# Optimization experiments

Hardware: AMD Instinct MI355X
Metric: run time of the kernel (lower is better)

Reference implementation:

```python
import jax, jax.numpy as jnp
import numpy as np

B, C, N, T = 32, 32, 300, 64      # batch, residual/conv channels, nodes, seq_len
DIM, K, SKIP, GD = 40, 20, 64, 2  # node_dim, top-k (subgraph_size), skip_channels, gcn_depth
TANH_A, PROP_A = 3.0, 0.05
KSET = (2, 3, 6, 7)
TOUT = T - (KSET[-1] - 1)          # 58: time length after dilated inception (dilation=1)


def conv2d(x, w, b):
    y = jax.lax.conv_general_dilated(x, w, (1, 1), 'VALID', dimension_numbers=('NCHW', 'OIHW', 'NCHW'))
    return y + b[None, :, None, None]


def setup_inputs() -> dict:
    key = jax.random.key(0)
    ks = iter(jax.random.split(key, 48))
    def nrm(shape, s=1.0):
        return jax.random.normal(next(ks), shape, jnp.float32) * s
    inp = {
        'x': nrm((B, C, N, T)),
        'x_skip': nrm((B, SKIP, N, 1)),
        'idx': jnp.arange(N, dtype=jnp.int32),
        'emb1': nrm((N, DIM), 0.1), 'emb2': nrm((N, DIM), 0.1),
        'lin1_w': nrm((DIM, DIM), 0.15), 'lin1_b': jnp.zeros((DIM,), jnp.float32),
        'lin2_w': nrm((DIM, DIM), 0.15), 'lin2_b': jnp.zeros((DIM,), jnp.float32),
        'skip_w': nrm((SKIP, C, 1, TOUT), 0.05), 'skip_b': jnp.zeros((SKIP,), jnp.float32),
        'mp1_w': nrm((C, (GD + 1) * C, 1, 1), 0.1), 'mp1_b': jnp.zeros((C,), jnp.float32),
        'mp2_w': nrm((C, (GD + 1) * C, 1, 1), 0.1), 'mp2_b': jnp.zeros((C,), jnp.float32),
        'ln_w': jnp.ones((C, N, TOUT), jnp.float32), 'ln_b': jnp.zeros((C, N, TOUT), jnp.float32),
    }
    for k in KSET:
        inp[f'fw{k}'] = nrm((C // 4, C, 1, k), 0.1); inp[f'fb{k}'] = jnp.zeros((C // 4,), jnp.float32)
        inp[f'gw{k}'] = nrm((C // 4, C, 1, k), 0.1); inp[f'gb{k}'] = jnp.zeros((C // 4,), jnp.float32)
    return inp


def _forward(x, x_skip, idx, emb1, emb2, lin1_w, lin1_b, lin2_w, lin2_b,
             fws, gws, skip_w, skip_b, mp1_w, mp1_b, mp2_w, mp2_b, ln_w, ln_b):
    # --- GraphConstructor: learned sparse adjacency via tanh/relu/top-k/scatter ---
    n1 = jnp.tanh(TANH_A * (emb1[idx] @ lin1_w.T + lin1_b))
    n2 = jnp.tanh(TANH_A * (emb2[idx] @ lin2_w.T + lin2_b))
    a = n1 @ n2.T - n2 @ n1.T
    A = jax.nn.relu(jnp.tanh(TANH_A * a))
    _, cols = jax.lax.top_k(A, K)                               # [N, K] per-row top-k indices
    mask = jnp.zeros_like(A).at[jnp.arange(N)[:, None], cols].set(1.0)
    A = A * mask
    # --- DilatedInception filter/gate (Conv2d kernel (1,k), crop to shortest) ---
    Xf = jnp.tanh(jnp.concatenate([conv2d(x, w, b)[..., -TOUT:] for w, b in fws], axis=1))
    Xg = jax.nn.sigmoid(jnp.concatenate([conv2d(x, w, b)[..., -TOUT:] for w, b in gws], axis=1))
    X = Xf * Xg                                                 # dropout is identity (training=False)
    X_skip_out = conv2d(X, skip_w, skip_b) + x_skip             # [B, SKIP, N, 1]
    # --- MixProp graph diffusion over A and A^T ---
    def mixprop(Xin, Adj, w, b):
        Ah = Adj + jnp.eye(N, dtype=Adj.dtype)
        Ah = Ah / Ah.sum(1)[:, None]                            # row-normalize
        H, hops = Xin, [Xin]
        for _ in range(GD):
            H = PROP_A * Xin + (1.0 - PROP_A) * jnp.einsum('bcwt,vw->bcvt', H, Ah)
            hops.append(H)
        return conv2d(jnp.concatenate(hops, axis=1), w, b)      # 1x1 conv: (GD+1)*C -> C
    X = mixprop(X, A, mp1_w, mp1_b) + mixprop(X, A.T, mp2_w, mp2_b)
    X = X + x[..., -TOUT:]
    # --- LayerNorm over (C, N, TOUT) with node-indexed affine ---
    mu = X.mean(axis=(1, 2, 3), keepdims=True)
    var = ((X - mu) ** 2).mean(axis=(1, 2, 3), keepdims=True)
    Xn = (X - mu) * jax.lax.rsqrt(var + 1e-5)
    X = Xn * ln_w[:, idx, :][None] + ln_b[:, idx, :][None]
    return X, X_skip_out


def reference(x, x_skip, idx, emb1, emb2, lin1_w, lin1_b, lin2_w, lin2_b,
              fw2, fb2, fw3, fb3, fw6, fb6, fw7, fb7,
              gw2, gb2, gw3, gb3, gw6, gb6, gw7, gb7,
              skip_w, skip_b, mp1_w, mp1_b, mp2_w, mp2_b, ln_w, ln_b):
    fws = [(fw2, fb2), (fw3, fb3), (fw6, fb6), (fw7, fb7)]
    gws = [(gw2, gb2), (gw3, gb3), (gw6, gb6), (gw7, gb7)]
    return _forward(x, x_skip, idx, emb1, emb2, lin1_w, lin1_b, lin2_w, lin2_b,
                    fws, gws, skip_w, skip_b, mp1_w, mp1_b, mp2_w, mp2_b, ln_w, ln_b)
```

## Files before the change

### kernel.cpp

```cpp
#include <hip/hip_runtime.h>
#include <hip/hip_bf16.h>
#include <math.h>

typedef __hip_bfloat16 bf16;
typedef __attribute__((ext_vector_type(8))) short bf16x8;
typedef __attribute__((ext_vector_type(4))) float f32x4;

#define NB 32
#define NC 32
#define NNODE 300
#define NT 64
#define NDIM 40
#define KTOP 20
#define NSKIP 64
#define NTOUT 58
#define SLAB 17400
#define BSLAB 556800
#define XEL 17817600
#define PSLAB 2048
#define BPSLAB 614400
#define XPEL 19660800

__device__ __forceinline__ float b2f(bf16 v){ return __bfloat162float(v); }
__device__ __forceinline__ bf16 f2b(float v){ return __float2bfloat16(v); }
__device__ __forceinline__ float fsig(float x){ return 1.0f/(1.0f + __expf(-x)); }
__device__ __forceinline__ float ftanh(float x){ return 2.0f*fsig(2.0f*x) - 1.0f; }

__device__ __forceinline__ unsigned short bbits(float v){
  bf16 h = f2b(v); unsigned short s; __builtin_memcpy(&s, &h, 2); return s;
}

__device__ __forceinline__ void fma8(float acc[8], uint4 d, float vv){
  acc[0] = fmaf(vv, __uint_as_float(d.x << 16),          acc[0]);
  acc[1] = fmaf(vv, __uint_as_float(d.x & 0xffff0000u),  acc[1]);
  acc[2] = fmaf(vv, __uint_as_float(d.y << 16),          acc[2]);
  acc[3] = fmaf(vv, __uint_as_float(d.y & 0xffff0000u),  acc[3]);
  acc[4] = fmaf(vv, __uint_as_float(d.z << 16),          acc[4]);
  acc[5] = fmaf(vv, __uint_as_float(d.z & 0xffff0000u),  acc[5]);
  acc[6] = fmaf(vv, __uint_as_float(d.w << 16),          acc[6]);
  acc[7] = fmaf(vv, __uint_as_float(d.w & 0xffff0000u),  acc[7]);
}

__device__ __forceinline__ void unp8(float f[8], uint4 d){
  f[0] = __uint_as_float(d.x << 16); f[1] = __uint_as_float(d.x & 0xffff0000u);
  f[2] = __uint_as_float(d.y << 16); f[3] = __uint_as_float(d.y & 0xffff0000u);
  f[4] = __uint_as_float(d.z << 16); f[5] = __uint_as_float(d.z & 0xffff0000u);
  f[6] = __uint_as_float(d.w << 16); f[7] = __uint_as_float(d.w & 0xffff0000u);
}

__device__ __forceinline__ uint4 pack8(const float f[8]){
  uint4 d;
  d.x = (unsigned)bbits(f[0]) | ((unsigned)bbits(f[1]) << 16);
  d.y = (unsigned)bbits(f[2]) | ((unsigned)bbits(f[3]) << 16);
  d.z = (unsigned)bbits(f[4]) | ((unsigned)bbits(f[5]) << 16);
  d.w = (unsigned)bbits(f[6]) | ((unsigned)bbits(f[7]) << 16);
  return d;
}

__device__ __forceinline__ void bv_swz(int bid, int& b, int& v){
  int xcd = bid & 7, i = bid >> 3;
  int nb = xcd*1200 + i;
  b = nb / NNODE; v = nb - b*NNODE;
}

__global__ void k_nodes(const float* __restrict__ emb1, const float* __restrict__ emb2,
                        const float* __restrict__ l1w, const float* __restrict__ l1b,
                        const float* __restrict__ l2w, const float* __restrict__ l2b,
                        const int* __restrict__ idxp,
                        float* __restrict__ n1, float* __restrict__ n2){
  int i = blockIdx.x; int d = threadIdx.x;
  if (d >= NDIM) return;
  int r = idxp[i];
  float a1 = l1b[d], a2 = l2b[d];
  for (int k=0;k<NDIM;++k){
    a1 = fmaf(emb1[r*NDIM+k], l1w[d*NDIM+k], a1);
    a2 = fmaf(emb2[r*NDIM+k], l2w[d*NDIM+k], a2);
  }
  n1[i*NDIM+d] = tanhf(3.0f*a1);
  n2[i*NDIM+d] = tanhf(3.0f*a2);
}

__global__ void __launch_bounds__(64) k_adjrow(const float* __restrict__ n1,
                                               const float* __restrict__ n2,
                                               float* __restrict__ Am){
  int i = blockIdx.x; int lane = threadIdx.x;
  __shared__ float rowo[NNODE];
  __shared__ float rowv[NNODE];
  __shared__ int   sel[NNODE];
  for (int j=lane;j<NNODE;j+=64){
    float a = 0.f;
    #pragma unroll
    for (int k=0;k<NDIM;++k){
      float a1 = n1[i*NDIM+k], a2 = n2[i*NDIM+k];
      a = fmaf(a1, n2[j*NDIM+k], a);
      a = fmaf(-a2, n1[j*NDIM+k], a);
    }
    float v = tanhf(3.0f*a);
    v = v > 0.f ? v : 0.f;
    rowo[j]=v; rowv[j]=v; sel[j]=0;
  }
  __syncthreads();
  for (int it=0; it<KTOP; ++it){
    float best = -1.f; int bi = 0x7fffffff;
    for (int j=lane;j<NNODE;j+=64){
      float v = rowv[j];
      if (v > best){ best=v; bi=j; }
    }
    #pragma unroll
    for (int off=32; off; off>>=1){
      float ov = __shfl_xor(best, off);
      int   oi = __shfl_xor(bi, off);
      if (ov > best || (ov == best && oi < bi)){ best=ov; bi=oi; }
    }
    if (lane==0){ sel[bi]=1; rowv[bi]=-2.f; }
    __syncthreads();
  }
  for (int j=lane;j<NNODE;j+=64)
    Am[i*NNODE+j] = sel[j] ? rowo[j] : 0.f;
}

__global__ void __launch_bounds__(64) k_csr(const float* __restrict__ Am,
                                            int* __restrict__ aidx, float* __restrict__ aval,
                                            int* __restrict__ acnt){
  int r = blockIdx.x; int lane = threadIdx.x;
  int v = (r < NNODE) ? r : r - NNODE;
  int*   ip = aidx + r*304;
  float* vp = aval + r*304;
  if (lane==0){ ip[0]=v; vp[0]=1.0f; }
  int cnt = 1; float s = 1.0f;
  for (int base=0; base<NNODE; base+=64){
    int j = base + lane; float val = 0.f; bool p = false;
    if (j < NNODE){
      val = (r < NNODE) ? Am[v*NNODE + j] : Am[j*NNODE + v];
      p = val > 0.f;
    }
    unsigned long long m = __ballot(p);
    int pre = __popcll(m & ((1ull << lane) - 1ull));
    if (p){ ip[cnt+pre]=j; vp[cnt+pre]=val; }
    cnt += __popcll(m);
    float vs = p ? val : 0.f;
    #pragma unroll
    for (int off=32; off; off>>=1) vs += __shfl_xor(vs, off);
    s += vs;
  }
  for (int e=lane; e<cnt; e+=64) vp[e] = vp[e] / s;
  if (lane==0) acnt[r]=cnt;
}

__global__ void k_wpack2(const float* __restrict__ fw2,const float* __restrict__ fw3,
                         const float* __restrict__ fw6,const float* __restrict__ fw7,
                         const float* __restrict__ gw2,const float* __restrict__ gw3,
                         const float* __restrict__ gw6,const float* __restrict__ gw7,
                         const float* __restrict__ fb2,const float* __restrict__ fb3,
                         const float* __restrict__ fb6,const float* __restrict__ fb7,
                         const float* __restrict__ gb2,const float* __restrict__ gb3,
                         const float* __restrict__ gb6,const float* __restrict__ gb7,
                         bf16* __restrict__ wfA, float* __restrict__ biasPk){
  int T = blockIdx.x*blockDim.x + threadIdx.x;
  if (T < 14336){
    int j = T & 7;
    int q = T >> 3;
    int l = q & 63; q >>= 6;
    int ks = q % 7, mt = q / 7;
    int m = mt*16 + (l & 15);
    int k = ks*32 + (l >> 4)*8 + j;
    int c = m >> 1, path = m & 1;
    int cls = c >> 3, o = c & 7;
    int ic = k / 7, d = k - ic*7;
    int kk = (cls==0) ? 2 : (cls==1) ? 3 : (cls==2) ? 6 : 7;
    int tp = d - (7 - kk);
    float val = 0.f;
    if (tp >= 0){
      const float* w = (path==0)
        ? (cls==0?fw2:cls==1?fw3:cls==2?fw6:fw7)
        : (cls==0?gw2:cls==1?gw3:cls==2?gw6:gw7);
      val = w[(o*NC + ic)*kk + tp];
    }
    wfA[T] = f2b(val);
  } else if (T < 14336 + 32){
    int c = T - 14336;
    int cls = c >> 3, o = c & 7;
    const float* fb = cls==0?fb2:cls==1?fb3:cls==2?fb6:fb7;
    const float* gb = cls==0?gb2:cls==1?gb3:cls==2?gb6:gb7;
    biasPk[c*2]   = fb[o];
    biasPk[c*2+1] = gb[o];
  }
}

__global__ void k_wprepM(const float* __restrict__ m1w, const float* __restrict__ m2w,
                         const float* __restrict__ m1b, const float* __restrict__ m2b,
                         bf16* __restrict__ pkB0, bf16* __restrict__ pkB1,
                         float* __restrict__ biasSum){
  int id = blockIdx.x*blockDim.x + threadIdx.x;
  if (id < 3072){
    int j = id & 7, l = (id >> 3) & 63, q = id >> 9;
    int ks = q % 3, nt = q / 3;
    int k = ks*32 + (l >> 4)*8 + j;
    int c = nt*16 + (l & 15);
    float val = m1w[c*96 + k] + (k < 32 ? m2w[c*96 + k] : 0.f);
    pkB0[id] = f2b(val);
  } else if (id < 5120){
    int id2 = id - 3072;
    int j = id2 & 7, l = (id2 >> 3) & 63, q = id2 >> 9;
    int ks = q & 1, nt = q >> 1;
    int k = ks*32 + (l >> 4)*8 + j;
    int c = nt*16 + (l & 15);
    pkB1[id2] = f2b(m2w[c*96 + 32 + k]);
  } else if (id < 5152){
    int c = id - 5120;
    biasSum[c] = m1b[c] + m2b[c];
  }
}

__global__ void k_wTb(const float* __restrict__ sw, bf16* __restrict__ wTb){
  int id = blockIdx.x*blockDim.x + threadIdx.x;
  if (id >= 131072) return;
  int j = id & 7, l = (id >> 3) & 63, q = id >> 9;
  int ks = q & 63, nt = q >> 6;
  int k = ks*32 + (l >> 4)*8 + j;
  int t = k >> 5, c = k & 31;
  int sc = nt*16 + (l & 15);
  float val = (t < NTOUT) ? sw[sc*1856 + c*NTOUT + t] : 0.f;
  wTb[id] = f2b(val);
}

__global__ void __launch_bounds__(256) k_incepM(const float* __restrict__ x,
    const bf16* __restrict__ wfA, const float* __restrict__ biasPk,
    bf16* __restrict__ Xp){
  __shared__ bf16 xsb[32*72];
  __shared__ uint4 xim2[28*64];
  int b, n; bv_swz(blockIdx.x, b, n);
  int bn = b*NNODE + n;
  int tid = threadIdx.x;
  {
    int c = tid >> 3, t0 = (tid & 7)*8;
    const float* src = x + ((size_t)(b*NC + c)*NNODE + n)*NT + t0;
    float4 v0 = *reinterpret_cast<const float4*>(src);
    float4 v1 = *reinterpret_cast<const float4*>(src + 4);
    float f[8] = {v0.x,v0.y,v0.z,v0.w,v1.x,v1.y,v1.z,v1.w};
    *reinterpret_cast<uint4*>(&xsb[c*72 + t0]) = pack8(f);
    if ((tid & 7) == 7)
      *reinterpret_cast<uint4*>(&xsb[c*72 + 64]) = make_uint4(0,0,0,0);
  }
  __syncthreads();
  #pragma unroll
  for (int i=0;i<7;++i){
    int pr = tid + i*256;
    int kb = pr >> 6, t = pr & 63;
    int k0 = kb*8;
    int ic = k0 / 7, d = k0 - ic*7;
    unsigned sh[8];
    #pragma unroll
    for (int j=0;j<8;++j){
      sh[j] = *reinterpret_cast<const unsigned short*>(&xsb[ic*72 + t + d]);
      ++d; if (d == 7){ d = 0; ++ic; }
    }
    xim2[kb*64 + t] = make_uint4(sh[0]|(sh[1]<<16), sh[2]|(sh[3]<<16),
                                 sh[4]|(sh[5]<<16), sh[6]|(sh[7]<<16));
  }
  __syncthreads();
  int lane = tid & 63;
  int mt = __builtin_amdgcn_readfirstlane(tid >> 6);
  bf16x8 wA[7];
  #pragma unroll
  for (int ks=0; ks<7; ++ks)
    wA[ks] = *reinterpret_cast<const bf16x8*>(wfA + (size_t)((mt*7 + ks)*64 + lane)*8);
  int g = lane >> 4;
  int c0 = mt*8 + 2*g;
  float4 bias2 = *reinterpret_cast<const float4*>(biasPk + c0*2);
  #pragma unroll
  for (int nt=0; nt<4; ++nt){
    int t = (lane & 15) + nt*16;
    f32x4 acc = {0.f, 0.f, 0.f, 0.f};
    #pragma unroll
    for (int ks=0; ks<7; ++ks){
      bf16x8 bfr = __builtin_bit_cast(bf16x8, xim2[(ks*4 + g)*64 + t]);
      acc = __builtin_amdgcn_mfma_f32_16x16x32_bf16(wA[ks], bfr, acc, 0, 0, 0);
    }
    bool act = t < NTOUT;
    float X0 = act ? (ftanh(acc[0] + bias2.x) * fsig(acc[1] + bias2.y)) : 0.f;
    float X1 = act ? (ftanh(acc[2] + bias2.z) * fsig(acc[3] + bias2.w)) : 0.f;
    unsigned pv = (unsigned)bbits(X0) | ((unsigned)bbits(X1) << 16);
    *reinterpret_cast<unsigned*>(Xp + (size_t)bn*PSLAB + t*32 + c0) = pv;
  }
}

__global__ void __launch_bounds__(256) k_skipM(const bf16* __restrict__ Xp, const bf16* __restrict__ wTb,
      const float* __restrict__ skip_b, const float* __restrict__ x_skip, float* __restrict__ out){
  int bn0 = blockIdx.x * 16;
  int tid = threadIdx.x, lane = tid & 63;
  int nt = __builtin_amdgcn_readfirstlane(tid >> 6);
  int g = lane >> 4, col = lane & 15;
  const bf16* aptr = Xp + (size_t)(bn0 + col)*PSLAB + g*8;
  const bf16* bptr = wTb + ((size_t)nt*64*64 + lane)*8;
  f32x4 acc = {0.f, 0.f, 0.f, 0.f};
  #pragma unroll 4
  for (int ks=0; ks<64; ++ks){
    bf16x8 aF = *reinterpret_cast<const bf16x8*>(aptr + ks*32);
    bf16x8 bF = *reinterpret_cast<const bf16x8*>(bptr + (size_t)ks*512);
    acc = __builtin_amdgcn_mfma_f32_16x16x32_bf16(aF, bF, acc, 0, 0, 0);
  }
  int sc = nt*16 + col;
  float sb = skip_b[sc];
  #pragma unroll
  for (int r=0;r<4;++r){
    int bn = bn0 + g*4 + r;
    int b = bn / NNODE, n = bn - b*NNODE;
    size_t so = (size_t)b*NSKIP*NNODE + (size_t)sc*NNODE + n;
    out[(size_t)XEL + so] = acc[r] + sb + x_skip[so];
  }
}

__global__ void __launch_bounds__(256) k_prop(const bf16* __restrict__ Xp, bf16* __restrict__ HA,
    const int* __restrict__ aidx, const float* __restrict__ aval, const int* __restrict__ acnt,
    int rowoff){
  __shared__ int   sidx[304];
  __shared__ float sval[304];
  int b, v; bv_swz(blockIdx.x, b, v);
  int r = rowoff + v;
  int cnt = acnt[r];
  for (int e = threadIdx.x; e < cnt; e += 256){
    sidx[e] = aidx[r*304 + e] * PSLAB;
    sval[e] = aval[r*304 + e];
  }
  __syncthreads();
  int t = threadIdx.x >> 2, cb = threadIdx.x & 3;
  int off = t*32 + cb*8;
  const bf16* base = Xp + (size_t)b*BPSLAB + off;
  float acc[8] = {0,0,0,0,0,0,0,0};
  #pragma unroll 2
  for (int j=0;j<cnt;++j){
    uint4 d = *reinterpret_cast<const uint4*>(base + sidx[j]);
    fma8(acc, d, sval[j]);
  }
  size_t own = (size_t)b*BPSLAB + (size_t)v*PSLAB + off;
  uint4 dx = *reinterpret_cast<const uint4*>(Xp + own);
  float xf[8]; unp8(xf, dx);
  float h[8];
  #pragma unroll
  for (int k=0;k<8;++k) h[k] = fmaf(0.95f, acc[k], 0.05f*xf[k]);
  *reinterpret_cast<uint4*>(HA + own) = pack8(h);
}

__global__ void __launch_bounds__(256) k_fuse(const bf16* __restrict__ Xp, const bf16* __restrict__ HA,
    float* __restrict__ out, const float* __restrict__ x,
    const int* __restrict__ aidx, const float* __restrict__ aval, const int* __restrict__ acnt,
    const bf16* __restrict__ pkB, const float* __restrict__ biasSum,
    int rowoff, int side){
  __shared__ int   sidx[304];
  __shared__ float sval[304];
  __shared__ uint4 h2T4[256];
  int b, v; bv_swz(blockIdx.x, b, v);
  int r = rowoff + v;
  int cnt = acnt[r];
  for (int e = threadIdx.x; e < cnt; e += 256){
    sidx[e] = aidx[r*304 + e] * PSLAB;
    sval[e] = aval[r*304 + e];
  }
  __syncthreads();
  int tid = threadIdx.x;
  size_t bbase = (size_t)b*BPSLAB;
  size_t vbase = bbase + (size_t)v*PSLAB;
  {
    int t = tid >> 2, cb = tid & 3;
    int off = t*32 + cb*8;
    const bf16* base = HA + bbase + off;
    float acc[8] = {0,0,0,0,0,0,0,0};
    #pragma unroll 2
    for (int j=0;j<cnt;++j){
      uint4 d = *reinterpret_cast<const uint4*>(base + sidx[j]);
      fma8(acc, d, sval[j]);
    }
    uint4 dx = *reinterpret_cast<const uint4*>(Xp + vbase + off);
    float xf[8]; unp8(xf, dx);
    float h[8];
    #pragma unroll
    for (int k=0;k<8;++k) h[k] = fmaf(0.95f, acc[k], 0.05f*xf[k]);
    h2T4[t*4 + cb] = pack8(h);
  }
  __syncthreads();
  int lane = tid & 63;
  int mt = __builtin_amdgcn_readfirstlane(tid >> 6);
  int g = lane >> 4, col = lane & 15;
  int tRow = mt*16 + col;
  const bf16x8* h2p = reinterpret_cast<const bf16x8*>(h2T4);
  bf16x8 aF0, aF1, aF2;
  if (side == 0){
    aF0 = *reinterpret_cast<const bf16x8*>(Xp + vbase + tRow*32 + g*8);
    aF1 = *reinterpret_cast<const bf16x8*>(HA + vbase + tRow*32 + g*8);
    aF2 = h2p[tRow*4 + g];
  } else {
    aF0 = *reinterpret_cast<const bf16x8*>(HA + vbase + tRow*32 + g*8);
    aF1 = h2p[tRow*4 + g];
    aF2 = aF1;
  }
  int t0 = mt*16 + g*4;
  #pragma unroll
  for (int nt=0; nt<2; ++nt){
    int c_out = nt*16 + col;
    f32x4 acc;
    if (side == 0){
      float bv = biasSum[c_out];
      acc = (f32x4){bv, bv, bv, bv};
      bf16x8 w0 = *reinterpret_cast<const bf16x8*>(pkB + (size_t)((nt*3+0)*64 + lane)*8);
      bf16x8 w1 = *reinterpret_cast<const bf16x8*>(pkB + (size_t)((nt*3+1)*64 + lane)*8);
      bf16x8 w2 = *reinterpret_cast<const bf16x8*>(pkB + (size_t)((nt*3+2)*64 + lane)*8);
      acc = __builtin_amdgcn_mfma_f32_16x16x32_bf16(aF0, w0, acc, 0, 0, 0);
      acc = __builtin_amdgcn_mfma_f32_16x16x32_bf16(aF1, w1, acc, 0, 0, 0);
      acc = __builtin_amdgcn_mfma_f32_16x16x32_bf16(aF2, w2, acc, 0, 0, 0);
      float* po = out + ((size_t)(b*NC + c_out)*NNODE + v)*NTOUT + t0;
      if (t0 <= 54){
        *reinterpret_cast<float2*>(po)     = make_float2(acc[0], acc[1]);
        *reinterpret_cast<float2*>(po + 2) = make_float2(acc[2], acc[3]);
      } else if (t0 == 56){
        *reinterpret_cast<float2*>(po)     = make_float2(acc[0], acc[1]);
      }
    } else {
      acc = (f32x4){0.f, 0.f, 0.f, 0.f};
      bf16x8 w0 = *reinterpret_cast<const bf16x8*>(pkB + (size_t)((nt*2+0)*64 + lane)*8);
      bf16x8 w1 = *reinterpret_cast<const bf16x8*>(pkB + (size_t)((nt*2+1)*64 + lane)*8);
      acc = __builtin_amdgcn_mfma_f32_16x16x32_bf16(aF0, w0, acc, 0, 0, 0);
      acc = __builtin_amdgcn_mfma_f32_16x16x32_bf16(aF1, w1, acc, 0, 0, 0);
      float* po = out + ((size_t)(b*NC + c_out)*NNODE + v)*NTOUT + t0;
      const float* rx = x + ((size_t)(b*NC + c_out)*NNODE + v)*NT + 6 + t0;
      if (t0 <= 54){
        float2 o0 = *reinterpret_cast<const float2*>(po);
        float2 o1 = *reinterpret_cast<const float2*>(po + 2);
        float2 r0 = *reinterpret_cast<const float2*>(rx);
        float2 r1 = *reinterpret_cast<const float2*>(rx + 2);
        *reinterpret_cast<float2*>(po)     = make_float2(o0.x + acc[0] + r0.x, o0.y + acc[1] + r0.y);
        *reinterpret_cast<float2*>(po + 2) = make_float2(o1.x + acc[2] + r1.x, o1.y + acc[3] + r1.y);
      } else if (t0 == 56){
        float2 o0 = *reinterpret_cast<const float2*>(po);
        float2 r0 = *reinterpret_cast<const float2*>(rx);
        *reinterpret_cast<float2*>(po)     = make_float2(o0.x + acc[0] + r0.x, o0.y + acc[1] + r0.y);
      }
    }
  }
}

__global__ void __launch_bounds__(256) k_lnstat(const float* __restrict__ out, double* __restrict__ part){
  int blk = blockIdx.x; int b = blk >> 3, seg = blk & 7;
  const float* p = out + (size_t)b*BSLAB;
  int start = seg*69600, end = start + 69600;
  double s = 0.0, s2 = 0.0;
  for (int i = start + threadIdx.x; i < end; i += 256){
    double v = (double)p[i]; s += v; s2 += v*v;
  }
  #pragma unroll
  for (int off=32; off; off>>=1){ s += __shfl_down(s, off); s2 += __shfl_down(s2, off); }
  __shared__ double ls[4], ls2[4];
  int lane = threadIdx.x & 63, w = threadIdx.x >> 6;
  if (lane==0){ ls[w]=s; ls2[w]=s2; }
  __syncthreads();
  if (threadIdx.x==0){
    double a=0.0, a2=0.0;
    for (int i=0;i<4;++i){ a+=ls[i]; a2+=ls2[i]; }
    part[blk*2]=a; part[blk*2+1]=a2;
  }
}

__global__ void k_lnfin(const double* __restrict__ part, float* __restrict__ stats){
  int b = threadIdx.x; if (b >= 32) return;
  double s=0.0, s2=0.0;
  for (int seg=0; seg<8; ++seg){ s += part[(b*8+seg)*2]; s2 += part[(b*8+seg)*2+1]; }
  double n = (double)BSLAB;
  double mean = s/n;
  double var = s2/n - mean*mean;
  stats[b*2]   = (float)mean;
  stats[b*2+1] = (float)(1.0/sqrt(var + 1e-5));
}

__global__ void __launch_bounds__(256) k_lnapply(float* __restrict__ out, const float* __restrict__ stats,
        const float* __restrict__ lnw, const float* __restrict__ lnb, const int* __restrict__ idxp){
  int o = blockIdx.x*256 + threadIdx.x;
  int t = o % NTOUT; int v = (o / NTOUT) % NNODE; int c = (o / SLAB) % NC; int b = o / BSLAB;
  float mean = stats[b*2], rstd = stats[b*2+1];
  int vn = idxp[v];
  float wv = lnw[((size_t)c*NNODE + vn)*NTOUT + t];
  float bv = lnb[((size_t)c*NNODE + vn)*NTOUT + t];
  float vx = out[o];
  out[o] = (vx - mean)*rstd*wv + bv;
}

extern "C" void kernel_launch(void* const* d_in, const int* in_sizes, int n_in,
                              void* d_out, int out_size, void* d_ws, size_t ws_size,
                              hipStream_t stream) {
  (void)in_sizes; (void)n_in; (void)out_size; (void)ws_size;
  const float* x     = (const float*)d_in[0];
  const float* xskip = (const float*)d_in[1];
  const int*   idxp  = (const int*)d_in[2];
  const float* emb1  = (const float*)d_in[3];
  const float* emb2  = (const float*)d_in[4];
  const float* l1w   = (const float*)d_in[5];
  const float* l1b   = (const float*)d_in[6];
  const float* l2w   = (const float*)d_in[7];
  const float* l2b   = (const float*)d_in[8];
  const float* skw   = (const float*)d_in[9];
  const float* skb   = (const float*)d_in[10];
  const float* m1w   = (const float*)d_in[11];
  const float* m1b   = (const float*)d_in[12];
  const float* m2w   = (const float*)d_in[13];
  const float* m2b   = (const float*)d_in[14];
  const float* lnw   = (const float*)d_in[15];
  const float* lnb   = (const float*)d_in[16];
  const float* fw2=(const float*)d_in[17]; const float* fb2=(const float*)d_in[18];
  const float* gw2=(const float*)d_in[19]; const float* gb2=(const float*)d_in[20];
  const float* fw3=(const float*)d_in[21]; const float* fb3=(const float*)d_in[22];
  const float* gw3=(const float*)d_in[23]; const float* gb3=(const float*)d_in[24];
  const float* fw6=(const float*)d_in[25]; const float* fb6=(const float*)d_in[26];
  const float* gw6=(const float*)d_in[27]; const float* gb6=(const float*)d_in[28];
  const float* fw7=(const float*)d_in[29]; const float* fb7=(const float*)d_in[30];
  const float* gw7=(const float*)d_in[31]; const float* gb7=(const float*)d_in[32];
  float* out = (float*)d_out;

  char* wsbase = (char*)d_ws;
  size_t cur = 0;
  auto alloc = [&](size_t bytes)->char*{
    char* p = wsbase + cur;
    cur = (cur + bytes + 255) & ~(size_t)255;
    return p;
  };
  bf16*  Xp   = (bf16*) alloc((size_t)XPEL*2);
  bf16*  HA   = (bf16*) alloc((size_t)XPEL*2);
  float* n1   = (float*)alloc(12000*4);
  float* n2   = (float*)alloc(12000*4);
  float* Am   = (float*)alloc(90000*4);
  int*   aidx = (int*)  alloc(600*304*4);
  float* aval = (float*)alloc(600*304*4);
  int*   acnt = (int*)  alloc(600*4);
  bf16*  wTb  = (bf16*) alloc(131072*2);
  bf16*  wfA  = (bf16*) alloc(14336*2);
  float* biasPk = (float*)alloc(64*4);
  bf16*  pkB0 = (bf16*) alloc(3072*2);
  bf16*  pkB1 = (bf16*) alloc(2048*2);
  float* biasSum = (float*)alloc(32*4);
  double* part = (double*)alloc(256*2*8);
  float* stats = (float*)alloc(64*4);

  k_nodes <<<NNODE, 64, 0, stream>>>(emb1, emb2, l1w, l1b, l2w, l2b, idxp, n1, n2);
  k_adjrow<<<NNODE, 64, 0, stream>>>(n1, n2, Am);
  k_csr   <<<2*NNODE, 64, 0, stream>>>(Am, aidx, aval, acnt);

  k_wpack2<<<57, 256, 0, stream>>>(fw2,fw3,fw6,fw7, gw2,gw3,gw6,gw7,
                                   fb2,fb3,fb6,fb7, gb2,gb3,gb6,gb7, wfA, biasPk);
  k_wprepM<<<21, 256, 0, stream>>>(m1w, m2w, m1b, m2b, pkB0, pkB1, biasSum);
  k_wTb   <<<512, 256, 0, stream>>>(skw, wTb);

  k_incepM<<<NB*NNODE, 256, 0, stream>>>(x, wfA, biasPk, Xp);

  k_skipM<<<(NB*NNODE)/16, 256, 0, stream>>>(Xp, wTb, skb, xskip, out);

  k_prop<<<NB*NNODE, 256, 0, stream>>>(Xp, HA, aidx, aval, acnt, 0);
  k_fuse<<<NB*NNODE, 256, 0, stream>>>(Xp, HA, out, x, aidx, aval, acnt, pkB0, biasSum, 0, 0);

  k_prop<<<NB*NNODE, 256, 0, stream>>>(Xp, HA, aidx, aval, acnt, NNODE);
  k_fuse<<<NB*NNODE, 256, 0, stream>>>(Xp, HA, out, x, aidx, aval, acnt, pkB1, biasSum, NNODE, 1);

  k_lnstat<<<256, 256, 0, stream>>>(out, part);
  k_lnfin<<<1, 32, 0, stream>>>(part, stats);
  k_lnapply<<<XEL/256, 256, 0, stream>>>(out, stats, lnw, lnb, idxp);
}
```

Baseline: 454.6 us.

## Replace sparse CSR propagation with dense MFMA hop matrices and fuse LN stats

Drops the CSR gather-based two-hop mixprop. It precomputes dense normalized propagation matrices for one and two hops (including the squared adjacency with the residual mixing folded in) in MFMA-packed bf16, then applies them to the node dimension with a tiled MFMA GEMM kernel. The two fuse kernels are split into hop-independent variants, and the LayerNorm statistics are accumulated with atomics inside the second fuse kernel, which removes the separate stats pass. This trades sparse gathers for dense tensor-core work on a 300x300 matrix. It adds rounding of the precomputed two-hop matrix to bf16, float partial sums before the double atomics, and an extra H buffer.

```diff
diff --git a/kernel.cpp b/kernel.cpp
--- a/kernel.cpp
+++ b/kernel.cpp
@@ -30,17 +30,6 @@
   bf16 h = f2b(v); unsigned short s; __builtin_memcpy(&s, &h, 2); return s;
 }
 
-__device__ __forceinline__ void fma8(float acc[8], uint4 d, float vv){
-  acc[0] = fmaf(vv, __uint_as_float(d.x << 16),          acc[0]);
-  acc[1] = fmaf(vv, __uint_as_float(d.x & 0xffff0000u),  acc[1]);
-  acc[2] = fmaf(vv, __uint_as_float(d.y << 16),          acc[2]);
-  acc[3] = fmaf(vv, __uint_as_float(d.y & 0xffff0000u),  acc[3]);
-  acc[4] = fmaf(vv, __uint_as_float(d.z << 16),          acc[4]);
-  acc[5] = fmaf(vv, __uint_as_float(d.z & 0xffff0000u),  acc[5]);
-  acc[6] = fmaf(vv, __uint_as_float(d.w << 16),          acc[6]);
-  acc[7] = fmaf(vv, __uint_as_float(d.w & 0xffff0000u),  acc[7]);
-}
-
 __device__ __forceinline__ void unp8(float f[8], uint4 d){
   f[0] = __uint_as_float(d.x << 16); f[1] = __uint_as_float(d.x & 0xffff0000u);
   f[2] = __uint_as_float(d.y << 16); f[3] = __uint_as_float(d.y & 0xffff0000u);
@@ -119,32 +108,50 @@
     Am[i*NNODE+j] = sel[j] ? rowo[j] : 0.f;
 }
 
-__global__ void __launch_bounds__(64) k_csr(const float* __restrict__ Am,
-                                            int* __restrict__ aidx, float* __restrict__ aval,
-                                            int* __restrict__ acnt){
-  int r = blockIdx.x; int lane = threadIdx.x;
-  int v = (r < NNODE) ? r : r - NNODE;
-  int*   ip = aidx + r*304;
-  float* vp = aval + r*304;
-  if (lane==0){ ip[0]=v; vp[0]=1.0f; }
-  int cnt = 1; float s = 1.0f;
-  for (int base=0; base<NNODE; base+=64){
-    int j = base + lane; float val = 0.f; bool p = false;
-    if (j < NNODE){
-      val = (r < NNODE) ? Am[v*NNODE + j] : Am[j*NNODE + v];
-      p = val > 0.f;
-    }
-    unsigned long long m = __ballot(p);
-    int pre = __popcll(m & ((1ull << lane) - 1ull));
-    if (p){ ip[cnt+pre]=j; vp[cnt+pre]=val; }
-    cnt += __popcll(m);
-    float vs = p ? val : 0.f;
-    #pragma unroll
-    for (int off=32; off; off>>=1) vs += __shfl_xor(vs, off);
-    s += vs;
-  }
-  for (int e=lane; e<cnt; e+=64) vp[e] = vp[e] / s;
-  if (lane==0) acnt[r]=cnt;
+__global__ void __launch_bounds__(64) k_norm(const float* __restrict__ Am, float* __restrict__ Ah){
+  int r = blockIdx.x;
+  int side = r >= 304; int v = side ? r - 304 : r;
+  float* dst = Ah + (size_t)(side ? 304*304 : 0) + v*304;
+  int lane = threadIdx.x;
+  if (v >= NNODE){
+    for (int w=lane; w<304; w+=64) dst[w] = 0.f;
+    return;
+  }
+  float s = 0.f;
+  for (int w=lane; w<NNODE; w+=64)
+    s += side ? Am[w*NNODE + v] : Am[v*NNODE + w];
+  #pragma unroll
+  for (int off=32; off; off>>=1) s += __shfl_xor(s, off);
+  float inv = 1.0f/(s + 1.0f);
+  for (int w=lane; w<304; w+=64){
+    float a = (w < NNODE) ? (side ? Am[w*NNODE + v] : Am[v*NNODE + w]) : 0.f;
+    if (w == v) a += 1.0f;
+    dst[w] = a*inv;
+  }
+}
+
+__global__ void k_mpk(const float* __restrict__ Ah, bf16* __restrict__ Mpk){
+  int id = blockIdx.x*blockDim.x + threadIdx.x;
+  if (id >= 4*320*320) return;
+  int pm = id / (320*320);
+  int rem = id % (320*320);
+  int v = rem / 320, w = rem % 320;
+  int s = pm >> 1, m = pm & 1;
+  float val = 0.f;
+  if (v < 304 && w < 304){
+    const float* A = Ah + (size_t)s*304*304;
+    float a = A[v*304 + w];
+    if (m == 0){
+      val = 0.95f*a + (v==w ? 0.05f : 0.f);
+    } else {
+      float d = 0.f;
+      for (int u=0; u<304; ++u) d = fmaf(A[v*304 + u], A[u*304 + w], d);
+      val = 0.9025f*d + 0.0475f*a + (v==w ? 0.05f : 0.f);
+    }
+  }
+  int vt16 = v >> 4, lv = v & 15, ks = w >> 5, g = (w >> 3) & 3, j = w & 7;
+  int lane = g*16 + lv;
+  Mpk[(((size_t)(pm*20 + vt16)*10 + ks)*64 + lane)*8 + j] = f2b(val);
 }
 
 __global__ void k_wpack2(const float* __restrict__ fw2,const float* __restrict__ fw3,
@@ -195,17 +202,20 @@
   if (id < 3072){
     int j = id & 7, l = (id >> 3) & 63, q = id >> 9;
     int ks = q % 3, nt = q / 3;
-    int k = ks*32 + (l >> 4)*8 + j;
+    int k = (l >> 4)*8 + j;
     int c = nt*16 + (l & 15);
-    float val = m1w[c*96 + k] + (k < 32 ? m2w[c*96 + k] : 0.f);
+    float val;
+    if      (ks == 0) val = m1w[c*96 + k] + m2w[c*96 + k];
+    else if (ks == 1) val = m1w[c*96 + 32 + k];
+    else              val = m1w[c*96 + 64 + k];
     pkB0[id] = f2b(val);
   } else if (id < 5120){
     int id2 = id - 3072;
     int j = id2 & 7, l = (id2 >> 3) & 63, q = id2 >> 9;
     int ks = q & 1, nt = q >> 1;
-    int k = ks*32 + (l >> 4)*8 + j;
+    int k = (l >> 4)*8 + j;
     int c = nt*16 + (l & 15);
-    pkB1[id2] = f2b(m2w[c*96 + 32 + k]);
+    pkB1[id2] = f2b(ks==0 ? m2w[c*96 + 32 + k] : m2w[c*96 + 64 + k]);
   } else if (id < 5152){
     int c = id - 5120;
     biasSum[c] = m1b[c] + m2b[c];
@@ -311,159 +321,171 @@
   }
 }
 
-__global__ void __launch_bounds__(256) k_prop(const bf16* __restrict__ Xp, bf16* __restrict__ HA,
-    const int* __restrict__ aidx, const float* __restrict__ aval, const int* __restrict__ acnt,
-    int rowoff){
-  __shared__ int   sidx[304];
-  __shared__ float sval[304];
+__global__ void __launch_bounds__(256) k_hop(const bf16* __restrict__ Xp,
+    const bf16* __restrict__ Mpk, bf16* __restrict__ H1, bf16* __restrict__ H2, int pass){
+  __shared__ uint4 bst4[4*130];
+  __shared__ __align__(16) unsigned short outT[64*136];
+  int bid = blockIdx.x;
+  int xcd = bid & 7, i = bid >> 3;
+  int nb = xcd*640 + i;
+  int b = nb / 160; int r = nb - b*160;
+  int m = r / 80; r -= m*80;
+  int vt = r >> 4; int ctt = r & 15;
+  int ct0 = ctt*128, v0 = vt*64;
+  int tid = threadIdx.x, lane = tid & 63;
+  int mt = __builtin_amdgcn_readfirstlane(tid >> 6);
+  int g = lane >> 4, col = lane & 15;
+  const bf16* xb = Xp + (size_t)b*BPSLAB;
+  const bf16* mbase = Mpk + (((size_t)((pass*2 + m)*20 + vt*4 + mt)*10)*64 + lane)*8;
+  f32x4 acc[8];
+  #pragma unroll
+  for (int nt=0; nt<8; ++nt) acc[nt] = (f32x4){0.f,0.f,0.f,0.f};
+  unsigned short* pb = reinterpret_cast<unsigned short*>(bst4);
+  for (int ks=0; ks<10; ++ks){
+    __syncthreads();
+    {
+      int wl = tid >> 3, e = tid & 7;
+      int w = ks*32 + wl;
+      #pragma unroll
+      for (int h=0; h<2; ++h){
+        int ctl = e*8 + h*64;
+        uint4 d = (w < NNODE) ? *reinterpret_cast<const uint4*>(xb + (size_t)w*PSLAB + ct0 + ctl)
+                              : make_uint4(0,0,0,0);
+        unsigned short u[8] = {
+          (unsigned short)(d.x & 0xffff), (unsigned short)(d.x >> 16),
+          (unsigned short)(d.y & 0xffff), (unsigned short)(d.y >> 16),
+          (unsigned short)(d.z & 0xffff), (unsigned short)(d.z >> 16),
+          (unsigned short)(d.w & 0xffff), (unsigned short)(d.w >> 16)};
+        int base = ((wl >> 3)*130 + ctl)*8 + (wl & 7);
+        #pragma unroll
+        for (int j=0;j<8;++j) pb[base + j*8] = u[j];
+      }
+    }
+    __syncthreads();
+    bf16x8 aF = *reinterpret_cast<const bf16x8*>(mbase + (size_t)ks*512);
+    #pragma unroll
+    for (int nt=0; nt<8; ++nt){
+      bf16x8 bF = __builtin_bit_cast(bf16x8, bst4[g*130 + nt*16 + col]);
+      acc[nt] = __builtin_amdgcn_mfma_f32_16x16x32_bf16(aF, bF, acc[nt], 0, 0, 0);
+    }
+  }
+  __syncthreads();
+  #pragma unroll
+  for (int nt=0; nt<8; ++nt){
+    #pragma unroll
+    for (int r4=0; r4<4; ++r4)
+      outT[(mt*16 + g*4 + r4)*136 + nt*16 + col] = bbits(acc[nt][r4]);
+  }
+  __syncthreads();
+  bf16* Hout = (m == 0) ? H1 : H2;
+  {
+    int vl = tid >> 2, e = tid & 3;
+    int v = v0 + vl;
+    if (v < NNODE){
+      bf16* dst = Hout + (size_t)b*BPSLAB + (size_t)v*PSLAB + ct0;
+      #pragma unroll
+      for (int h=0; h<4; ++h){
+        int ctl = e*32 + h*8;
+        uint4 d = *reinterpret_cast<const uint4*>(outT + vl*136 + ctl);
+        *reinterpret_cast<uint4*>(dst + ctl) = d;
+      }
+    }
+  }
+}
+
+__global__ void __launch_bounds__(256) k_fuse0(const bf16* __restrict__ Xp,
+    const bf16* __restrict__ H1, const bf16* __restrict__ H2,
+    float* __restrict__ out, const bf16* __restrict__ pkB, const float* __restrict__ biasSum){
   int b, v; bv_swz(blockIdx.x, b, v);
-  int r = rowoff + v;
-  int cnt = acnt[r];
-  for (int e = threadIdx.x; e < cnt; e += 256){
-    sidx[e] = aidx[r*304 + e] * PSLAB;
-    sval[e] = aval[r*304 + e];
-  }
-  __syncthreads();
-  int t = threadIdx.x >> 2, cb = threadIdx.x & 3;
-  int off = t*32 + cb*8;
-  const bf16* base = Xp + (size_t)b*BPSLAB + off;
-  float acc[8] = {0,0,0,0,0,0,0,0};
-  #pragma unroll 2
-  for (int j=0;j<cnt;++j){
-    uint4 d = *reinterpret_cast<const uint4*>(base + sidx[j]);
-    fma8(acc, d, sval[j]);
-  }
-  size_t own = (size_t)b*BPSLAB + (size_t)v*PSLAB + off;
-  uint4 dx = *reinterpret_cast<const uint4*>(Xp + own);
-  float xf[8]; unp8(xf, dx);
-  float h[8];
-  #pragma unroll
-  for (int k=0;k<8;++k) h[k] = fmaf(0.95f, acc[k], 0.05f*xf[k]);
-  *reinterpret_cast<uint4*>(HA + own) = pack8(h);
-}
-
-__global__ void __launch_bounds__(256) k_fuse(const bf16* __restrict__ Xp, const bf16* __restrict__ HA,
-    float* __restrict__ out, const float* __restrict__ x,
-    const int* __restrict__ aidx, const float* __restrict__ aval, const int* __restrict__ acnt,
-    const bf16* __restrict__ pkB, const float* __restrict__ biasSum,
-    int rowoff, int side){
-  __shared__ int   sidx[304];
-  __shared__ float sval[304];
-  __shared__ uint4 h2T4[256];
-  int b, v; bv_swz(blockIdx.x, b, v);
-  int r = rowoff + v;
-  int cnt = acnt[r];
-  for (int e = threadIdx.x; e < cnt; e += 256){
-    sidx[e] = aidx[r*304 + e] * PSLAB;
-    sval[e] = aval[r*304 + e];
-  }
-  __syncthreads();
-  int tid = threadIdx.x;
-  size_t bbase = (size_t)b*BPSLAB;
-  size_t vbase = bbase + (size_t)v*PSLAB;
-  {
-    int t = tid >> 2, cb = tid & 3;
-    int off = t*32 + cb*8;
-    const bf16* base = HA + bbase + off;
-    float acc[8] = {0,0,0,0,0,0,0,0};
-    #pragma unroll 2
-    for (int j=0;j<cnt;++j){
-      uint4 d = *reinterpret_cast<const uint4*>(base + sidx[j]);
-      fma8(acc, d, sval[j]);
-    }
-    uint4 dx = *reinterpret_cast<const uint4*>(Xp + vbase + off);
-    float xf[8]; unp8(xf, dx);
-    float h[8];
-    #pragma unroll
-    for (int k=0;k<8;++k) h[k] = fmaf(0.95f, acc[k], 0.05f*xf[k]);
-    h2T4[t*4 + cb] = pack8(h);
-  }
-  __syncthreads();
-  int lane = tid & 63;
+  size_t vbase = (size_t)b*BPSLAB + (size_t)v*PSLAB;
+  int tid = threadIdx.x, lane = tid & 63;
   int mt = __builtin_amdgcn_readfirstlane(tid >> 6);
   int g = lane >> 4, col = lane & 15;
   int tRow = mt*16 + col;
-  const bf16x8* h2p = reinterpret_cast<const bf16x8*>(h2T4);
-  bf16x8 aF0, aF1, aF2;
-  if (side == 0){
-    aF0 = *reinterpret_cast<const bf16x8*>(Xp + vbase + tRow*32 + g*8);
-    aF1 = *reinterpret_cast<const bf16x8*>(HA + vbase + tRow*32 + g*8);
-    aF2 = h2p[tRow*4 + g];
-  } else {
-    aF0 = *reinterpret_cast<const bf16x8*>(HA + vbase + tRow*32 + g*8);
-    aF1 = h2p[tRow*4 + g];
-    aF2 = aF1;
-  }
+  bf16x8 aX = *reinterpret_cast<const bf16x8*>(Xp + vbase + tRow*32 + g*8);
+  bf16x8 a1 = *reinterpret_cast<const bf16x8*>(H1 + vbase + tRow*32 + g*8);
+  bf16x8 a2 = *reinterpret_cast<const bf16x8*>(H2 + vbase + tRow*32 + g*8);
   int t0 = mt*16 + g*4;
   #pragma unroll
   for (int nt=0; nt<2; ++nt){
     int c_out = nt*16 + col;
-    f32x4 acc;
-    if (side == 0){
-      float bv = biasSum[c_out];
-      acc = (f32x4){bv, bv, bv, bv};
-      bf16x8 w0 = *reinterpret_cast<const bf16x8*>(pkB + (size_t)((nt*3+0)*64 + lane)*8);
-      bf16x8 w1 = *reinterpret_cast<const bf16x8*>(pkB + (size_t)((nt*3+1)*64 + lane)*8);
-      bf16x8 w2 = *reinterpret_cast<const bf16x8*>(pkB + (size_t)((nt*3+2)*64 + lane)*8);
-      acc = __builtin_amdgcn_mfma_f32_16x16x32_bf16(aF0, w0, acc, 0, 0, 0);
-      acc = __builtin_amdgcn_mfma_f32_16x16x32_bf16(aF1, w1, acc, 0, 0, 0);
-      acc = __builtin_amdgcn_mfma_f32_16x16x32_bf16(aF2, w2, acc, 0, 0, 0);
-      float* po = out + ((size_t)(b*NC + c_out)*NNODE + v)*NTOUT + t0;
-      if (t0 <= 54){
-        *reinterpret_cast<float2*>(po)     = make_float2(acc[0], acc[1]);
-        *reinterpret_cast<float2*>(po + 2) = make_float2(acc[2], acc[3]);
-      } else if (t0 == 56){
-        *reinterpret_cast<float2*>(po)     = make_float2(acc[0], acc[1]);
-      }
-    } else {
-      acc = (f32x4){0.f, 0.f, 0.f, 0.f};
-      bf16x8 w0 = *reinterpret_cast<const bf16x8*>(pkB + (size_t)((nt*2+0)*64 + lane)*8);
-      bf16x8 w1 = *reinterpret_cast<const bf16x8*>(pkB + (size_t)((nt*2+1)*64 + lane)*8);
-      acc = __builtin_amdgcn_mfma_f32_16x16x32_bf16(aF0, w0, acc, 0, 0, 0);
-      acc = __builtin_amdgcn_mfma_f32_16x16x32_bf16(aF1, w1, acc, 0, 0, 0);
-      float* po = out + ((size_t)(b*NC + c_out)*NNODE + v)*NTOUT + t0;
-      const float* rx = x + ((size_t)(b*NC + c_out)*NNODE + v)*NT + 6 + t0;
-      if (t0 <= 54){
-        float2 o0 = *reinterpret_cast<const float2*>(po);
-        float2 o1 = *reinterpret_cast<const float2*>(po + 2);
-        float2 r0 = *reinterpret_cast<const float2*>(rx);
-        float2 r1 = *reinterpret_cast<const float2*>(rx + 2);
-        *reinterpret_cast<float2*>(po)     = make_float2(o0.x + acc[0] + r0.x, o0.y + acc[1] + r0.y);
-        *reinterpret_cast<float2*>(po + 2) = make_float2(o1.x + acc[2] + r1.x, o1.y + acc[3] + r1.y);
-      } else if (t0 == 56){
-        float2 o0 = *reinterpret_cast<const float2*>(po);
-        float2 r0 = *reinterpret_cast<const float2*>(rx);
-        *reinterpret_cast<float2*>(po)     = make_float2(o0.x + acc[0] + r0.x, o0.y + acc[1] + r0.y);
-      }
-    }
-  }
-}
-
-__global__ void __launch_bounds__(256) k_lnstat(const float* __restrict__ out, double* __restrict__ part){
-  int blk = blockIdx.x; int b = blk >> 3, seg = blk & 7;
-  const float* p = out + (size_t)b*BSLAB;
-  int start = seg*69600, end = start + 69600;
-  double s = 0.0, s2 = 0.0;
-  for (int i = start + threadIdx.x; i < end; i += 256){
-    double v = (double)p[i]; s += v; s2 += v*v;
-  }
-  #pragma unroll
-  for (int off=32; off; off>>=1){ s += __shfl_down(s, off); s2 += __shfl_down(s2, off); }
-  __shared__ double ls[4], ls2[4];
-  int lane = threadIdx.x & 63, w = threadIdx.x >> 6;
-  if (lane==0){ ls[w]=s; ls2[w]=s2; }
+    float bv = biasSum[c_out];
+    f32x4 acc = {bv, bv, bv, bv};
+    bf16x8 w0 = *reinterpret_cast<const bf16x8*>(pkB + (size_t)((nt*3+0)*64 + lane)*8);
+    bf16x8 w1 = *reinterpret_cast<const bf16x8*>(pkB + (size_t)((nt*3+1)*64 + lane)*8);
+    bf16x8 w2 = *reinterpret_cast<const bf16x8*>(pkB + (size_t)((nt*3+2)*64 + lane)*8);
+    acc = __builtin_amdgcn_mfma_f32_16x16x32_bf16(aX, w0, acc, 0, 0, 0);
+    acc = __builtin_amdgcn_mfma_f32_16x16x32_bf16(a1, w1, acc, 0, 0, 0);
+    acc = __builtin_amdgcn_mfma_f32_16x16x32_bf16(a2, w2, acc, 0, 0, 0);
+    float* po = out + ((size_t)(b*NC + c_out)*NNODE + v)*NTOUT + t0;
+    if (t0 <= 54){
+      *reinterpret_cast<float2*>(po)     = make_float2(acc[0], acc[1]);
+      *reinterpret_cast<float2*>(po + 2) = make_float2(acc[2], acc[3]);
+    } else if (t0 == 56){
+      *reinterpret_cast<float2*>(po)     = make_float2(acc[0], acc[1]);
+    }
+  }
+}
+
+__global__ void __launch_bounds__(256) k_fuse1(const bf16* __restrict__ H1, const bf16* __restrict__ H2,
+    float* __restrict__ out, const float* __restrict__ x,
+    const bf16* __restrict__ pkB, double* __restrict__ part2){
+  __shared__ float redS[4], redS2[4];
+  int b, v; bv_swz(blockIdx.x, b, v);
+  size_t vbase = (size_t)b*BPSLAB + (size_t)v*PSLAB;
+  int tid = threadIdx.x, lane = tid & 63;
+  int mt = __builtin_amdgcn_readfirstlane(tid >> 6);
+  int g = lane >> 4, col = lane & 15;
+  int tRow = mt*16 + col;
+  bf16x8 a1 = *reinterpret_cast<const bf16x8*>(H1 + vbase + tRow*32 + g*8);
+  bf16x8 a2 = *reinterpret_cast<const bf16x8*>(H2 + vbase + tRow*32 + g*8);
+  int t0 = mt*16 + g*4;
+  float s = 0.f, s2 = 0.f;
+  #pragma unroll
+  for (int nt=0; nt<2; ++nt){
+    int c_out = nt*16 + col;
+    f32x4 acc = {0.f, 0.f, 0.f, 0.f};
+    bf16x8 w0 = *reinterpret_cast<const bf16x8*>(pkB + (size_t)((nt*2+0)*64 + lane)*8);
+    bf16x8 w1 = *reinterpret_cast<const bf16x8*>(pkB + (size_t)((nt*2+1)*64 + lane)*8);
+    acc = __builtin_amdgcn_mfma_f32_16x16x32_bf16(a1, w0, acc, 0, 0, 0);
+    acc = __builtin_amdgcn_mfma_f32_16x16x32_bf16(a2, w1, acc, 0, 0, 0);
+    float* po = out + ((size_t)(b*NC + c_out)*NNODE + v)*NTOUT + t0;
+    const float* rx = x + ((size_t)(b*NC + c_out)*NNODE + v)*NT + 6 + t0;
+    if (t0 <= 54){
+      float2 o0 = *reinterpret_cast<const float2*>(po);
+      float2 o1 = *reinterpret_cast<const float2*>(po + 2);
+      float2 r0 = *reinterpret_cast<const float2*>(rx);
+      float2 r1 = *reinterpret_cast<const float2*>(rx + 2);
+      float f0 = o0.x + acc[0] + r0.x, f1 = o0.y + acc[1] + r0.y;
+      float f2v = o1.x + acc[2] + r1.x, f3 = o1.y + acc[3] + r1.y;
+      *reinterpret_cast<float2*>(po)     = make_float2(f0, f1);
+      *reinterpret_cast<float2*>(po + 2) = make_float2(f2v, f3);
+      s  += f0 + f1 + f2v + f3;
+      s2 += f0*f0 + f1*f1 + f2v*f2v + f3*f3;
+    } else if (t0 == 56){
+      float2 o0 = *reinterpret_cast<const float2*>(po);
+      float2 r0 = *reinterpret_cast<const float2*>(rx);
+      float f0 = o0.x + acc[0] + r0.x, f1 = o0.y + acc[1] + r0.y;
+      *reinterpret_cast<float2*>(po) = make_float2(f0, f1);
+      s  += f0 + f1;
+      s2 += f0*f0 + f1*f1;
+    }
+  }
+  #pragma unroll
+  for (int o=32; o; o>>=1){ s += __shfl_down(s, o); s2 += __shfl_down(s2, o); }
+  if (lane == 0){ redS[mt] = s; redS2[mt] = s2; }
   __syncthreads();
-  if (threadIdx.x==0){
-    double a=0.0, a2=0.0;
-    for (int i=0;i<4;++i){ a+=ls[i]; a2+=ls2[i]; }
-    part[blk*2]=a; part[blk*2+1]=a2;
-  }
-}
-
-__global__ void k_lnfin(const double* __restrict__ part, float* __restrict__ stats){
+  if (tid == 0){
+    float as = redS[0]+redS[1]+redS[2]+redS[3];
+    float as2 = redS2[0]+redS2[1]+redS2[2]+redS2[3];
+    atomicAdd(&part2[b*2],   (double)as);
+    atomicAdd(&part2[b*2+1], (double)as2);
+  }
+}
+
+__global__ void k_lnfin(const double* __restrict__ part2, float* __restrict__ stats){
   int b = threadIdx.x; if (b >= 32) return;
-  double s=0.0, s2=0.0;
-  for (int seg=0; seg<8; ++seg){ s += part[(b*8+seg)*2]; s2 += part[(b*8+seg)*2+1]; }
+  double s = part2[b*2], s2 = part2[b*2+1];
   double n = (double)BSLAB;
   double mean = s/n;
   double var = s2/n - mean*mean;
@@ -522,25 +544,28 @@
     return p;
   };
   bf16*  Xp   = (bf16*) alloc((size_t)XPEL*2);
-  bf16*  HA   = (bf16*) alloc((size_t)XPEL*2);
+  bf16*  H1   = (bf16*) alloc((size_t)XPEL*2);
+  bf16*  H2   = (bf16*) alloc((size_t)XPEL*2);
   float* n1   = (float*)alloc(12000*4);
   float* n2   = (float*)alloc(12000*4);
   float* Am   = (float*)alloc(90000*4);
-  int*   aidx = (int*)  alloc(600*304*4);
-  float* aval = (float*)alloc(600*304*4);
-  int*   acnt = (int*)  alloc(600*4);
+  float* Ah   = (float*)alloc(2*304*304*4);
+  bf16*  Mpk  = (bf16*) alloc((size_t)4*20*10*64*8*2);
   bf16*  wTb  = (bf16*) alloc(131072*2);
   bf16*  wfA  = (bf16*) alloc(14336*2);
   float* biasPk = (float*)alloc(64*4);
   bf16*  pkB0 = (bf16*) alloc(3072*2);
   bf16*  pkB1 = (bf16*) alloc(2048*2);
   float* biasSum = (float*)alloc(32*4);
-  double* part = (double*)alloc(256*2*8);
+  double* part2 = (double*)alloc(64*8);
   float* stats = (float*)alloc(64*4);
+
+  hipMemsetAsync(part2, 0, 64*sizeof(double), stream);
 
   k_nodes <<<NNODE, 64, 0, stream>>>(emb1, emb2, l1w, l1b, l2w, l2b, idxp, n1, n2);
   k_adjrow<<<NNODE, 64, 0, stream>>>(n1, n2, Am);
-  k_csr   <<<2*NNODE, 64, 0, stream>>>(Am, aidx, aval, acnt);
+  k_norm  <<<608, 64, 0, stream>>>(Am, Ah);
+  k_mpk   <<<1600, 256, 0, stream>>>(Ah, Mpk);
 
   k_wpack2<<<57, 256, 0, stream>>>(fw2,fw3,fw6,fw7, gw2,gw3,gw6,gw7,
                                    fb2,fb3,fb6,fb7, gb2,gb3,gb6,gb7, wfA, biasPk);
@@ -551,13 +576,12 @@
 
   k_skipM<<<(NB*NNODE)/16, 256, 0, stream>>>(Xp, wTb, skb, xskip, out);
 
-  k_prop<<<NB*NNODE, 256, 0, stream>>>(Xp, HA, aidx, aval, acnt, 0);
-  k_fuse<<<NB*NNODE, 256, 0, stream>>>(Xp, HA, out, x, aidx, aval, acnt, pkB0, biasSum, 0, 0);
-
-  k_prop<<<NB*NNODE, 256, 0, stream>>>(Xp, HA, aidx, aval, acnt, NNODE);
-  k_fuse<<<NB*NNODE, 256, 0, stream>>>(Xp, HA, out, x, aidx, aval, acnt, pkB1, biasSum, NNODE, 1);
-
-  k_lnstat<<<256, 256, 0, stream>>>(out, part);
-  k_lnfin<<<1, 32, 0, stream>>>(part, stats);
+  k_hop  <<<5120, 256, 0, stream>>>(Xp, Mpk, H1, H2, 0);
+  k_fuse0<<<NB*NNODE, 256, 0, stream>>>(Xp, H1, H2, out, pkB0, biasSum);
+
+  k_hop  <<<5120, 256, 0, stream>>>(Xp, Mpk, H1, H2, 1);
+  k_fuse1<<<NB*NNODE, 256, 0, stream>>>(H1, H2, out, x, pkB1, part2);
+
+  k_lnfin<<<1, 32, 0, stream>>>(part2, stats);
   k_lnapply<<<XEL/256, 256, 0, stream>>>(out, stats, lnw, lnb, idxp);
 }
```

New measurement: 573.9 us. 26.3% more time.
